# Kernel tuning notes

Hardware: AMD Instinct MI355X
Metric: run time of the kernel (lower is better)

Reference implementation:

```python
import jax, jax.numpy as jnp
import numpy as np
from jax import lax

# ---- config (mirrors TrinityGuidance init kwargs) ----
GAMMA = 10.0        # LSE smoothing
M = 64              # RUDY grid size
THRESH = 1.0        # congestion threshold
SIGMA = 1.5         # gaussian smoothing sigma
K_SOFT = 2.0        # soft-bbox sigmoid sharpness
W_WL, W_CONG = 1.0, 0.5

B, V, P, NN, MP = 4, 20000, 400000, 50000, 32

# 4 rotation matrices (0/90/180/270 deg)
R_ALL = jnp.array([[[1, 0], [0, 1]],
                   [[0, -1], [1, 0]],
                   [[-1, 0], [0, -1]],
                   [[0, 1], [-1, 0]]], dtype=jnp.float32)


def _gauss_kernel(sigma):
    ksize = max(int(4 * sigma) | 1, 3)
    x = jnp.arange(ksize, dtype=jnp.float32) - ksize // 2
    g = jnp.exp(-x ** 2 / (2.0 * sigma ** 2))
    g2 = g[None, :] * g[:, None]
    return g2 / g2.sum()  # (k,k)


def setup_inputs() -> dict:
    key = jax.random.key(0)
    ks = jax.random.split(key, 7)
    positions = jax.random.uniform(ks[0], (B, V, 2), minval=-1.0, maxval=1.0)
    pin_to_macro = jax.random.randint(ks[1], (P,), 0, V)
    pin_offsets = jax.random.normal(ks[2], (P, 2)) * 0.01
    n2p = jax.random.randint(ks[3], (NN, MP), 0, P)
    # ragged nets: first cnt pins valid, rest padded with -1 (cnt in [2, MP])
    cnt = jax.random.randint(ks[4], (NN, 1), 2, MP + 1)
    net_to_pin = jnp.where(jnp.arange(MP)[None, :] < cnt, n2p, -1)
    rot_idx = jax.random.randint(ks[5], (B, V), 0, 4)
    rotation_onehot = jax.nn.one_hot(rot_idx, 4, dtype=jnp.float32)
    net_weights = jax.random.uniform(ks[6], (NN,), minval=0.5, maxval=1.5)
    return dict(positions=positions, net_to_pin=net_to_pin,
                pin_to_macro=pin_to_macro, pin_offsets=pin_offsets,
                rotation_onehot=rotation_onehot, net_weights=net_weights)


def _forward(positions, pin_offsets, rotation_onehot, net_weights,
             net_to_pin, pin_to_macro):
    # --- pin positions with rotated offsets ---
    macro_pos = positions[:, pin_to_macro, :]            # (B,P,2) gather
    macro_rot = rotation_onehot[:, pin_to_macro, :]      # (B,P,4)
    Rm = jnp.einsum('bpk,kij->bpij', macro_rot, R_ALL)   # (B,P,2,2)
    rotated = jnp.einsum('bpij,pj->bpi', Rm, pin_offsets)
    pin_pos = macro_pos + rotated                        # (B,P,2)

    valid = net_to_pin >= 0                              # (NN,MP)
    safe = jnp.maximum(net_to_pin, 0)
    net_pin_pos = pin_pos[:, safe, :]                    # (B,NN,MP,2)
    maskf = valid[None, :, :, None]
    masked_max = jnp.where(maskf, net_pin_pos, -1e9)
    masked_min = jnp.where(maskf, net_pin_pos, 1e9)

    # --- WA wirelength via masked double logsumexp per net ---
    gamma = jnp.float32(GAMMA)
    lse_max = jax.nn.logsumexp(gamma * masked_max, axis=2) / gamma   # (B,NN,2)
    lse_min = -jax.nn.logsumexp(-gamma * masked_min, axis=2) / gamma
    wl_per_net = (lse_max - lse_min).sum(-1)             # (B,NN)
    hpwl = (wl_per_net * net_weights[None, :]).sum(1)    # (B,)

    # --- RUDY congestion (separable soft-bbox, no (B,N,M,M) materialization) ---
    bbox_max = masked_max.max(axis=2)                    # (B,NN,2)
    bbox_min = masked_min.min(axis=2)
    bmax = (bbox_max + 1.0) * 0.5 * (M - 1)
    bmin = (bbox_min + 1.0) * 0.5 * (M - 1)
    x_min, y_min = bmin[..., 0:1], bmin[..., 1:2]        # (B,NN,1)
    x_max, y_max = bmax[..., 0:1], bmax[..., 1:2]
    g = jnp.arange(M, dtype=jnp.float32)[None, None, :]  # (1,1,M)
    in_x = jax.nn.sigmoid(K_SOFT * (g - x_min + 0.5)) * \
           jax.nn.sigmoid(K_SOFT * (x_max - g + 0.5))    # (B,NN,M)
    in_y = jax.nn.sigmoid(K_SOFT * (g - y_min + 0.5)) * \
           jax.nn.sigmoid(K_SOFT * (y_max - g + 0.5))    # (B,NN,M)
    bbox_size = jnp.maximum((x_max - x_min + 1.0) * (y_max - y_min + 1.0), 1.0)
    # rudy[b,i,j] = sum_n in_y[b,n,i] * in_x[b,n,j] / bbox_size[b,n]
    rudy = jnp.einsum('bni,bnj->bij', in_y / bbox_size, in_x)
    rudy = rudy[:, None, :, :]                           # (B,1,M,M)

    kernel = _gauss_kernel(SIGMA)                        # (k,k)
    pad = kernel.shape[-1] // 2
    rudy_smooth = lax.conv_general_dilated(
        rudy, kernel[None, None, :, :],
        window_strides=(1, 1), padding=[(pad, pad), (pad, pad)],
        dimension_numbers=('NCHW', 'OIHW', 'NCHW'))
    overflow = jax.nn.relu(rudy_smooth - THRESH)
    penalty = (overflow ** 2).sum(axis=(1, 2, 3))        # (B,)

    return W_WL * hpwl + W_CONG * penalty                # (B,)


def reference(positions, net_to_pin, pin_to_macro, pin_offsets,
              rotation_onehot, net_weights):
    return _forward(positions, pin_offsets, rotation_onehot, net_weights,
                    net_to_pin, pin_to_macro)
```

## Files before the change

kernel.cpp:

```cpp
#include <hip/hip_runtime.h>
#include <cstddef>

namespace {

constexpr int B = 4, V = 20000, P = 400000, NN = 50000, MP = 32;
constexpr float GAMMA = 10.0f, INV_GAMMA = 0.1f;
constexpr float KSOFT = 2.0f;
constexpr float THRESH = 1.0f;
constexpr float W_WL = 1.0f, W_CONG = 0.5f;
constexpr int BPB = 128;
constexpr int NET_GRID = BPB * B;
constexpr int GRPS = 7;
constexpr int NPW = GRPS * 16;
constexpr int A_SUBS = 196;
constexpr int A_GRID = A_SUBS * B;
constexpr int PREP_N = NN * MP;

typedef __attribute__((ext_vector_type(8)))  short bf16x8;
typedef __attribute__((ext_vector_type(16))) float f32x16;

__device__ __forceinline__ float fast_rcp(float x) { return __builtin_amdgcn_rcpf(x); }
__device__ __forceinline__ short f2bf(float f) {
    unsigned u = __float_as_uint(f);
    u += 0x7fffu + ((u >> 16) & 1u);
    return (short)(u >> 16);
}
template <int CTRL>
__device__ __forceinline__ float dpp_mov(float x, float id) {
    return __int_as_float(__builtin_amdgcn_update_dpp(
        __float_as_int(id), __float_as_int(x), CTRL, 0xf, 0xf, false));
}
__device__ __forceinline__ float rdlane(float x, int l) {
    return __int_as_float(__builtin_amdgcn_readlane(__float_as_int(x), l));
}
#define DPP5(x, OP, ID)                              \
    x = OP(x, dpp_mov<0x111>(x, ID));                \
    x = OP(x, dpp_mov<0x112>(x, ID));                \
    x = OP(x, dpp_mov<0x114>(x, ID));                \
    x = OP(x, dpp_mov<0x118>(x, ID));                \
    x = OP(x, dpp_mov<0x142>(x, ID));
__device__ __forceinline__ float op_add(float a, float b) { return a + b; }

__global__ void __launch_bounds__(256)
prep_kernel(const float* __restrict__ positions,
            const float* __restrict__ rot_onehot,
            float4* __restrict__ mac,
            const int* __restrict__ n2p,
            int* __restrict__ n2pT,
            float* __restrict__ zacc) {
    int i = blockIdx.x * blockDim.x + threadIdx.x;
    if (i < 2 * B) zacc[i] = 0.0f;
    if (i < B * V) {
        float2 pos = ((const float2*)positions)[i];
        float4 w = ((const float4*)rot_onehot)[i];
        mac[i] = make_float4(pos.x, pos.y, w.x - w.z, w.y - w.w);
    }
    if (i < PREP_N) {
        int n = i >> 5, j = i & 31;
        n2pT[j * NN + n] = n2p[i];
    }
}

__global__ void __launch_bounds__(256)
pin_pos_kernel(const float4* __restrict__ mac,
               const int* __restrict__ pin_to_macro,
               const float* __restrict__ pin_offsets,
               float* __restrict__ pin_pos) {
    int idx = blockIdx.x * blockDim.x + threadIdx.x;
    if (idx >= B * P / 2) return;
    int b = idx / (P / 2);
    int t = idx - b * (P / 2);
    int2 m2 = ((const int2*)pin_to_macro)[t];
    float4 o2 = ((const float4*)pin_offsets)[t];
    float4 md0 = mac[(size_t)b * V + m2.x];
    float4 md1 = mac[(size_t)b * V + m2.y];
    float4 r;
    r.x = md0.x + md0.z * o2.x - md0.w * o2.y;
    r.y = md0.y + md0.w * o2.x + md0.z * o2.y;
    r.z = md1.x + md1.z * o2.z - md1.w * o2.w;
    r.w = md1.y + md1.w * o2.z + md1.z * o2.w;
    ((float4*)pin_pos)[idx] = r;
}

__global__ void __launch_bounds__(256)
bbox_kernel(const float* __restrict__ pin_pos,
            const int* __restrict__ n2pT,
            const float* __restrict__ net_weights,
            float4* __restrict__ fac,
            float* __restrict__ hpwl) {
    __shared__ float hps[4];
    int blk = blockIdx.x;
    int xcd = blk & 7;
    int b = xcd >> 1;
    int sub = ((blk >> 3) << 1) | (xcd & 1);
    int tid = threadIdx.x;
    int wave = tid >> 6;
    int lane = tid & 63;

    int n = sub * 256 + wave * 64 + lane;
    bool inrange = n < NN;
    int nc = inrange ? n : (NN - 1);

    const float2* pp = (const float2*)(pin_pos + (size_t)b * P * 2);

    int pi[MP];
    #pragma unroll
    for (int j = 0; j < MP; ++j) pi[j] = n2pT[j * NN + nc];

    float2 q[MP];
    #pragma unroll
    for (int j = 0; j < MP; ++j) q[j] = pp[pi[j] >= 0 ? pi[j] : 0];

    float ex1 = 0.f, ex2 = 0.f, ey1 = 0.f, ey2 = 0.f;
    float vxmax = -1e30f, vxmin = 1e30f, vymax = -1e30f, vymin = 1e30f;
    #pragma unroll
    for (int j = 0; j < MP; ++j) {
        bool v = pi[j] >= 0;
        float e1x = __expf(GAMMA * q[j].x);
        float e1y = __expf(GAMMA * q[j].y);
        ex1 += v ? e1x : 0.f;
        ex2 += v ? fast_rcp(e1x) : 0.f;
        ey1 += v ? e1y : 0.f;
        ey2 += v ? fast_rcp(e1y) : 0.f;
        vxmax = fmaxf(vxmax, v ? q[j].x : -1e30f);
        vxmin = fminf(vxmin, v ? q[j].x :  1e30f);
        vymax = fmaxf(vymax, v ? q[j].y : -1e30f);
        vymin = fminf(vymin, v ? q[j].y :  1e30f);
    }
    float w = net_weights[nc];
    float wl = __logf(ex1 * ex2 * ey1 * ey2) * INV_GAMMA;
    float hp = inrange ? wl * w : 0.f;

    if (inrange) {
        float xmin = (vxmin + 1.0f) * 31.5f;
        float xmax = (vxmax + 1.0f) * 31.5f;
        float ymin = (vymin + 1.0f) * 31.5f;
        float ymax = (vymax + 1.0f) * 31.5f;
        float sz = fmaxf((xmax - xmin + 1.0f) * (ymax - ymin + 1.0f), 1.0f);
        float ux = __expf(fmaf( KSOFT, xmin, -32.5f * KSOFT));
        float wx = __expf(fmaf(-KSOFT, xmax,  31.5f * KSOFT));
        float uy = __expf(fmaf( KSOFT, ymin, -32.5f * KSOFT));
        float wy = __expf(fmaf(-KSOFT, ymax,  31.5f * KSOFT));
        float cx = fmaf(ux, wx, 1.0f);
        float cy = fmaf(uy, wy, 1.0f) * sz;
        float4* fp = fac + ((size_t)b * NN + n) * 2;
        fp[0] = make_float4(ux, wx, cx, 0.f);
        fp[1] = make_float4(uy * sz, wy * sz, cy, 0.f);
    }
    DPP5(hp, op_add, 0.0f);
    float tot = rdlane(hp, 31) + rdlane(hp, 63);
    if (lane == 0) hps[wave] = tot;
    __syncthreads();
    if (tid == 0) atomicAdd(&hpwl[b], hps[0] + hps[1] + hps[2] + hps[3]);
}

__global__ void __launch_bounds__(256)
rudy_kernel(const float4* __restrict__ fac,
            float* __restrict__ slabs) {
    __shared__ float lds4[4][4096];
    int x = blockIdx.x;
    int xcd = x & 7;
    int b = xcd >> 1;
    int sub = ((x >> 3) << 1) | (xcd & 1);
    int tid = threadIdx.x;
    int wave = tid >> 6;
    int lane = tid & 63;

    int s = sub * 4 + wave;
    int s0 = s * NPW;
    const float* ff = (const float*)(fac + (size_t)b * NN * 2);

    #pragma unroll
    for (int k = 0; k < 14; ++k) {
        int d = s0 * 8 + k * 64 + lane;
        lds4[wave][k * 64 + lane] = ff[d < NN * 8 ? d : 0];
    }
    const float4* st = (const float4*)lds4[wave];

    f32x16 acc00, acc01, acc10, acc11;
    #pragma unroll
    for (int r = 0; r < 16; ++r) { acc00[r] = 0.f; acc01[r] = 0.f; acc10[r] = 0.f; acc11[r] = 0.f; }

    int half8 = (lane >> 5) * 8;
    float g2 = (float)(lane & 31);

    float En0 = __expf(fmaf(-KSOFT, g2,  32.0f * KSOFT));
    float Ep0 = __expf(fmaf( KSOFT, g2, -32.0f * KSOFT));
    float EnH = __expf(-KSOFT * g2);
    float EpH = __expf( KSOFT * g2);

    if (s0 < NN) {
        float4 fbc[8], fyc[8];
        #pragma unroll
        for (int j = 0; j < 8; ++j) {
            fbc[j] = st[2 * (half8 + j)];
            fyc[j] = st[2 * (half8 + j) + 1];
        }
        #pragma unroll
        for (int grp = 0; grp < GRPS; ++grp) {
            float4 fbn[8], fyn[8];
            if (grp + 1 < GRPS) {
                #pragma unroll
                for (int j = 0; j < 8; ++j) {
                    fbn[j] = st[2 * ((grp + 1) * 16 + half8 + j)];
                    fyn[j] = st[2 * ((grp + 1) * 16 + half8 + j) + 1];
                }
            }
            int nb = s0 + grp * 16 + half8;
            bf16x8 A0, A1, B0, B1;
            #pragma unroll
            for (int j = 0; j < 8; ++j) {
                float4 fb = fbc[j];
                float4 fy = fyc[j];
                float okf = (nb + j < NN) ? 1.0f : 0.0f;
                float b0 = fast_rcp(fmaf(En0, fb.x, fmaf(Ep0, fb.y, fb.z)));
                float b1 = fast_rcp(fmaf(EnH, fb.x, fmaf(EpH, fb.y, fb.z)));
                float a0 = fast_rcp(fmaf(En0, fy.x, fmaf(Ep0, fy.y, fy.z))) * okf;
                float a1 = fast_rcp(fmaf(EnH, fy.x, fmaf(EpH, fy.y, fy.z))) * okf;
                A0[j] = f2bf(a0); A1[j] = f2bf(a1);
                B0[j] = f2bf(b0); B1[j] = f2bf(b1);
            }
            acc00 = __builtin_amdgcn_mfma_f32_32x32x16_bf16(A0, B0, acc00, 0, 0, 0);
            acc01 = __builtin_amdgcn_mfma_f32_32x32x16_bf16(A0, B1, acc01, 0, 0, 0);
            acc10 = __builtin_amdgcn_mfma_f32_32x32x16_bf16(A1, B0, acc10, 0, 0, 0);
            acc11 = __builtin_amdgcn_mfma_f32_32x32x16_bf16(A1, B1, acc11, 0, 0, 0);
            if (grp + 1 < GRPS) {
                #pragma unroll
                for (int j = 0; j < 8; ++j) { fbc[j] = fbn[j]; fyc[j] = fyn[j]; }
            }
        }
    }

    int col = lane & 31, rq = lane >> 5;
    float* wt = lds4[wave];
    #pragma unroll
    for (int r = 0; r < 16; ++r) {
        int row = (r & 3) + 8 * (r >> 2) + 4 * rq;
        wt[row * 64 + col]             = acc00[r];
        wt[row * 64 + col + 32]        = acc01[r];
        wt[(row + 32) * 64 + col]      = acc10[r];
        wt[(row + 32) * 64 + col + 32] = acc11[r];
    }
    __syncthreads();
    float* slab = slabs + ((size_t)b * BPB + sub) * 4096;
    for (int k = tid; k < 4096; k += 256)
        slab[k] = (lds4[0][k] + lds4[1][k]) + (lds4[2][k] + lds4[3][k]);
}

__global__ void __launch_bounds__(256)
rudy_reduce_kernel(const float* __restrict__ slabs, float* __restrict__ rudy) {
    int blk = blockIdx.x;
    int xcd = blk & 7;
    int b = xcd >> 1;
    int sub = ((blk >> 3) << 1) | (xcd & 1);
    int c = sub * 256 + threadIdx.x;
    const float* base = slabs + (size_t)b * BPB * 4096 + c;
    float a0 = 0.f, a1 = 0.f, a2 = 0.f, a3 = 0.f;
    #pragma unroll 4
    for (int s = 0; s < BPB; s += 4) {
        a0 += base[(size_t)(s + 0) * 4096];
        a1 += base[(size_t)(s + 1) * 4096];
        a2 += base[(size_t)(s + 2) * 4096];
        a3 += base[(size_t)(s + 3) * 4096];
    }
    rudy[b * 4096 + c] = (a0 + a1) + (a2 + a3);
}

__global__ void conv_penalty_kernel(const float* __restrict__ rudy,
                                    float* __restrict__ pen) {
    int blk = blockIdx.x;
    int b = blk >> 4, chunk = blk & 15;
    int r0 = chunk * 4;
    __shared__ float t2[10][64];
    int tid = threadIdx.x;
    for (int k = tid; k < 640; k += 256) {
        int r = k >> 6, c = k & 63, row = r0 - 3 + r;
        t2[r][c] = (row >= 0 && row < 64) ? rudy[b * 4096 + row * 64 + c] : 0.f;
    }
    __syncthreads();
    float g1[7];
    #pragma unroll
    for (int i = 0; i < 7; ++i) { float t = (float)(i - 3); g1[i] = __expf(-t * t / 4.5f); }
    float s1 = g1[0] + g1[1] + g1[2] + g1[3] + g1[4] + g1[5] + g1[6];
    float inv = fast_rcp(s1 * s1);
    int i = tid >> 6, j = tid & 63;
    float acc = 0.f;
    #pragma unroll
    for (int di = -3; di <= 3; ++di) {
        #pragma unroll
        for (int dj = -3; dj <= 3; ++dj) {
            int jj = j + dj;
            float val = (jj >= 0 && jj < 64) ? t2[i + 3 + di][jj] : 0.f;
            acc += g1[di + 3] * g1[dj + 3] * val;
        }
    }
    acc *= inv;
    float ov = acc - THRESH;
    float p = ov > 0.f ? ov * ov : 0.f;
    DPP5(p, op_add, 0.0f);
    float tot = rdlane(p, 31) + rdlane(p, 63);
    if ((tid & 63) == 0) atomicAdd(&pen[b], tot);
}

__global__ void finalize_kernel(const float* __restrict__ hpwl,
                                const float* __restrict__ pen,
                                float* __restrict__ out) {
    int i = threadIdx.x;
    if (i < B) out[i] = W_WL * hpwl[i] + W_CONG * pen[i];
}

}

extern "C" void kernel_launch(void* const* d_in, const int* in_sizes, int n_in,
                              void* d_out, int out_size, void* d_ws, size_t ws_size,
                              hipStream_t stream) {
    const float* positions    = (const float*)d_in[0];
    const int*   net_to_pin   = (const int*)d_in[1];
    const int*   pin_to_macro = (const int*)d_in[2];
    const float* pin_offsets  = (const float*)d_in[3];
    const float* rot_onehot   = (const float*)d_in[4];
    const float* net_weights  = (const float*)d_in[5];
    float* out = (float*)d_out;

    float*  pin_pos = (float*)d_ws;
    float*  rudy    = pin_pos + (size_t)B * P * 2;
    float*  hpwl    = rudy + (size_t)B * 64 * 64;
    float*  pen     = hpwl + B;
    float4* mac     = (float4*)(pen + B);
    float4* fac     = mac + (size_t)B * V;
    int*    n2pT    = (int*)(fac + (size_t)B * NN * 2);
    float*  slabs   = pin_pos;

    prep_kernel<<<(PREP_N + 255) / 256, 256, 0, stream>>>(
        positions, rot_onehot, mac, net_to_pin, n2pT, hpwl);
    pin_pos_kernel<<<(B * P / 2 + 255) / 256, 256, 0, stream>>>(
        mac, pin_to_macro, pin_offsets, pin_pos);
    bbox_kernel<<<A_GRID, 256, 0, stream>>>(pin_pos, n2pT, net_weights, fac, hpwl);
    rudy_kernel<<<NET_GRID, 256, 0, stream>>>(fac, slabs);
    rudy_reduce_kernel<<<64, 256, 0, stream>>>(slabs, rudy);
    conv_penalty_kernel<<<64, 256, 0, stream>>>(rudy, pen);
    finalize_kernel<<<1, 64, 0, stream>>>(hpwl, pen, out);
}
```

Baseline: 152.3 us.

## Fuse front prep kernels and tail reduce/conv/finalize kernels into fewer launches

Merges the prep and pin-position kernels into one front kernel that gathers positions and rotation one-hots directly instead of going through an intermediate per-macro table. Merges the slab reduction, Gaussian convolution/penalty and finalize into one tail kernel, with a last-block atomic counter writing the output. This removes three kernel launches and the intermediate rudy/mac buffers. In exchange, the tail recomputes slab sums for the halo rows (8 rows reduced per 2 output rows), half of each block's threads sit idle during the convolution, and the front kernel does scattered reads from two arrays instead of one packed float4.

```diff
diff --git a/kernel.cpp b/kernel.cpp
--- a/kernel.cpp
+++ b/kernel.cpp
@@ -15,6 +15,7 @@
 constexpr int A_SUBS = 196;
 constexpr int A_GRID = A_SUBS * B;
 constexpr int PREP_N = NN * MP;
+constexpr int TCH = 32;
 
 typedef __attribute__((ext_vector_type(8)))  short bf16x8;
 typedef __attribute__((ext_vector_type(16))) float f32x16;
@@ -42,44 +43,40 @@
 __device__ __forceinline__ float op_add(float a, float b) { return a + b; }
 
 __global__ void __launch_bounds__(256)
-prep_kernel(const float* __restrict__ positions,
-            const float* __restrict__ rot_onehot,
-            float4* __restrict__ mac,
-            const int* __restrict__ n2p,
-            int* __restrict__ n2pT,
-            float* __restrict__ zacc) {
+front_kernel(const float* __restrict__ positions,
+             const float* __restrict__ rot_onehot,
+             const int* __restrict__ pin_to_macro,
+             const float* __restrict__ pin_offsets,
+             const int* __restrict__ n2p,
+             int* __restrict__ n2pT,
+             float* __restrict__ pin_pos,
+             float* __restrict__ zacc,
+             int* __restrict__ cnt) {
     int i = blockIdx.x * blockDim.x + threadIdx.x;
     if (i < 2 * B) zacc[i] = 0.0f;
-    if (i < B * V) {
-        float2 pos = ((const float2*)positions)[i];
-        float4 w = ((const float4*)rot_onehot)[i];
-        mac[i] = make_float4(pos.x, pos.y, w.x - w.z, w.y - w.w);
+    if (i < B) cnt[i] = 0;
+    if (i < B * P / 2) {
+        int b = i / (P / 2);
+        int t = i - b * (P / 2);
+        int2 m2 = ((const int2*)pin_to_macro)[t];
+        float4 o2 = ((const float4*)pin_offsets)[t];
+        const float2* pos2 = (const float2*)positions + (size_t)b * V;
+        const float4* rot4 = (const float4*)rot_onehot + (size_t)b * V;
+        float2 p0 = pos2[m2.x], p1 = pos2[m2.y];
+        float4 w0 = rot4[m2.x], w1 = rot4[m2.y];
+        float c0 = w0.x - w0.z, s0 = w0.y - w0.w;
+        float c1 = w1.x - w1.z, s1 = w1.y - w1.w;
+        float4 r;
+        r.x = p0.x + c0 * o2.x - s0 * o2.y;
+        r.y = p0.y + s0 * o2.x + c0 * o2.y;
+        r.z = p1.x + c1 * o2.z - s1 * o2.w;
+        r.w = p1.y + s1 * o2.z + c1 * o2.w;
+        ((float4*)pin_pos)[i] = r;
     }
     if (i < PREP_N) {
         int n = i >> 5, j = i & 31;
         n2pT[j * NN + n] = n2p[i];
     }
-}
-
-__global__ void __launch_bounds__(256)
-pin_pos_kernel(const float4* __restrict__ mac,
-               const int* __restrict__ pin_to_macro,
-               const float* __restrict__ pin_offsets,
-               float* __restrict__ pin_pos) {
-    int idx = blockIdx.x * blockDim.x + threadIdx.x;
-    if (idx >= B * P / 2) return;
-    int b = idx / (P / 2);
-    int t = idx - b * (P / 2);
-    int2 m2 = ((const int2*)pin_to_macro)[t];
-    float4 o2 = ((const float4*)pin_offsets)[t];
-    float4 md0 = mac[(size_t)b * V + m2.x];
-    float4 md1 = mac[(size_t)b * V + m2.y];
-    float4 r;
-    r.x = md0.x + md0.z * o2.x - md0.w * o2.y;
-    r.y = md0.y + md0.w * o2.x + md0.z * o2.y;
-    r.z = md1.x + md1.z * o2.z - md1.w * o2.w;
-    r.w = md1.y + md1.w * o2.z + md1.z * o2.w;
-    ((float4*)pin_pos)[idx] = r;
 }
 
 __global__ void __launch_bounds__(256)
@@ -248,65 +245,75 @@
 }
 
 __global__ void __launch_bounds__(256)
-rudy_reduce_kernel(const float* __restrict__ slabs, float* __restrict__ rudy) {
+tail_kernel(const float* __restrict__ slabs,
+            const float* __restrict__ hpwl,
+            float* __restrict__ pen,
+            int* __restrict__ cnt,
+            float* __restrict__ out) {
     int blk = blockIdx.x;
     int xcd = blk & 7;
     int b = xcd >> 1;
     int sub = ((blk >> 3) << 1) | (xcd & 1);
-    int c = sub * 256 + threadIdx.x;
-    const float* base = slabs + (size_t)b * BPB * 4096 + c;
-    float a0 = 0.f, a1 = 0.f, a2 = 0.f, a3 = 0.f;
-    #pragma unroll 4
-    for (int s = 0; s < BPB; s += 4) {
-        a0 += base[(size_t)(s + 0) * 4096];
-        a1 += base[(size_t)(s + 1) * 4096];
-        a2 += base[(size_t)(s + 2) * 4096];
-        a3 += base[(size_t)(s + 3) * 4096];
-    }
-    rudy[b * 4096 + c] = (a0 + a1) + (a2 + a3);
-}
-
-__global__ void conv_penalty_kernel(const float* __restrict__ rudy,
-                                    float* __restrict__ pen) {
-    int blk = blockIdx.x;
-    int b = blk >> 4, chunk = blk & 15;
-    int r0 = chunk * 4;
-    __shared__ float t2[10][64];
+    int r0 = sub * 2;
+    __shared__ float t2[8][64];
     int tid = threadIdx.x;
-    for (int k = tid; k < 640; k += 256) {
-        int r = k >> 6, c = k & 63, row = r0 - 3 + r;
-        t2[r][c] = (row >= 0 && row < 64) ? rudy[b * 4096 + row * 64 + c] : 0.f;
+
+    for (int k = tid; k < 512; k += 256) {
+        int r = k >> 6, c = k & 63;
+        int row = r0 - 3 + r;
+        float v = 0.f;
+        if (row >= 0 && row < 64) {
+            const float* base = slabs + (size_t)b * BPB * 4096 + row * 64 + c;
+            float a0 = 0.f, a1 = 0.f, a2 = 0.f, a3 = 0.f;
+            #pragma unroll 4
+            for (int s = 0; s < BPB; s += 4) {
+                a0 += base[(size_t)(s + 0) * 4096];
+                a1 += base[(size_t)(s + 1) * 4096];
+                a2 += base[(size_t)(s + 2) * 4096];
+                a3 += base[(size_t)(s + 3) * 4096];
+            }
+            v = (a0 + a1) + (a2 + a3);
+        }
+        t2[r][c] = v;
     }
     __syncthreads();
+
     float g1[7];
     #pragma unroll
     for (int i = 0; i < 7; ++i) { float t = (float)(i - 3); g1[i] = __expf(-t * t / 4.5f); }
     float s1 = g1[0] + g1[1] + g1[2] + g1[3] + g1[4] + g1[5] + g1[6];
     float inv = fast_rcp(s1 * s1);
-    int i = tid >> 6, j = tid & 63;
-    float acc = 0.f;
-    #pragma unroll
-    for (int di = -3; di <= 3; ++di) {
+
+    float p = 0.f;
+    if (tid < 128) {
+        int i = tid >> 6, j = tid & 63;
+        float acc = 0.f;
         #pragma unroll
-        for (int dj = -3; dj <= 3; ++dj) {
-            int jj = j + dj;
-            float val = (jj >= 0 && jj < 64) ? t2[i + 3 + di][jj] : 0.f;
-            acc += g1[di + 3] * g1[dj + 3] * val;
-        }
-    }
-    acc *= inv;
-    float ov = acc - THRESH;
-    float p = ov > 0.f ? ov * ov : 0.f;
+        for (int di = -3; di <= 3; ++di) {
+            #pragma unroll
+            for (int dj = -3; dj <= 3; ++dj) {
+                int jj = j + dj;
+                float val = (jj >= 0 && jj < 64) ? t2[i + 3 + di][jj] : 0.f;
+                acc += g1[di + 3] * g1[dj + 3] * val;
+            }
+        }
+        acc *= inv;
+        float ov = acc - THRESH;
+        p = ov > 0.f ? ov * ov : 0.f;
+    }
     DPP5(p, op_add, 0.0f);
     float tot = rdlane(p, 31) + rdlane(p, 63);
     if ((tid & 63) == 0) atomicAdd(&pen[b], tot);
-}
-
-__global__ void finalize_kernel(const float* __restrict__ hpwl,
-                                const float* __restrict__ pen,
-                                float* __restrict__ out) {
-    int i = threadIdx.x;
-    if (i < B) out[i] = W_WL * hpwl[i] + W_CONG * pen[i];
+    __syncthreads();
+    if (tid == 0) {
+        __threadfence();
+        int old = atomicAdd(&cnt[b], 1);
+        if (old == TCH - 1) {
+            __threadfence();
+            float pv = atomicAdd(&pen[b], 0.0f);
+            out[b] = W_WL * hpwl[b] + W_CONG * pv;
+        }
+    }
 }
 
 }
@@ -323,21 +330,17 @@
     float* out = (float*)d_out;
 
     float*  pin_pos = (float*)d_ws;
-    float*  rudy    = pin_pos + (size_t)B * P * 2;
-    float*  hpwl    = rudy + (size_t)B * 64 * 64;
+    float*  hpwl    = pin_pos + (size_t)B * P * 2;
     float*  pen     = hpwl + B;
-    float4* mac     = (float4*)(pen + B);
-    float4* fac     = mac + (size_t)B * V;
+    int*    cnt     = (int*)(pen + B);
+    float4* fac     = (float4*)(cnt + B);
     int*    n2pT    = (int*)(fac + (size_t)B * NN * 2);
     float*  slabs   = pin_pos;
 
-    prep_kernel<<<(PREP_N + 255) / 256, 256, 0, stream>>>(
-        positions, rot_onehot, mac, net_to_pin, n2pT, hpwl);
-    pin_pos_kernel<<<(B * P / 2 + 255) / 256, 256, 0, stream>>>(
-        mac, pin_to_macro, pin_offsets, pin_pos);
+    front_kernel<<<(PREP_N + 255) / 256, 256, 0, stream>>>(
+        positions, rot_onehot, pin_to_macro, pin_offsets,
+        net_to_pin, n2pT, pin_pos, hpwl, cnt);
     bbox_kernel<<<A_GRID, 256, 0, stream>>>(pin_pos, n2pT, net_weights, fac, hpwl);
     rudy_kernel<<<NET_GRID, 256, 0, stream>>>(fac, slabs);
-    rudy_reduce_kernel<<<64, 256, 0, stream>>>(slabs, rudy);
-    conv_penalty_kernel<<<64, 256, 0, stream>>>(rudy, pen);
-    finalize_kernel<<<1, 64, 0, stream>>>(hpwl, pen, out);
-}
+    tail_kernel<<<TCH * B, 256, 0, stream>>>(slabs, hpwl, pen, cnt, out);
+}
```

Result: slower. 162.1 us (+6.4%).
